# Kernel optimization log

Hardware: AMD Instinct MI355X
Metric: run time of the kernel (lower is better)

The kernel has to match this reference:

```python
import jax, jax.numpy as jnp
import numpy as np

B, C, H = 64, 64, 32

def _pm_cross_pairs(ks):
    # Replicates PM_cross(2, ks): pairs (i, i+j) ordered by gap j=1..ks-1, then i.
    a, b = [], []
    for j in range(1, ks):
        for i in range(ks - j):
            a.append(i)
            b.append(i + j)
    return np.array(a, dtype=np.int32), np.array(b, dtype=np.int32)

def setup_inputs() -> dict:
    key = jax.random.key(0)
    k1, k2 = jax.random.split(key)
    ia, ib = _pm_cross_pairs(H)           # 496 pairs for H=32
    hk = ia.shape[0] + 2 * H              # 560
    x = jax.random.normal(k1, (B, C, H, H), dtype=jnp.float32)
    weight = 0.1 * jax.random.normal(k2, (C, H, hk, H), dtype=jnp.float32)
    return {"x": x, "weight": weight, "idx_a": jnp.asarray(ia), "idx_b": jnp.asarray(ib)}

def reference(x, weight, idx_a, idx_b):
    # cross-term products along last axis: [B,C,H,P]
    cross = x[..., idx_a] * x[..., idx_b]
    feat = jnp.concatenate([x, x * x, cross], axis=-1)  # [B,C,H,Hk]
    # per-(channel,row) grouped matmul
    return jnp.einsum('bcij,cijo->bcio', feat, weight)
```

## Files before the change

kernel.cpp:

```cpp
#include <hip/hip_runtime.h>

#define NB 64
#define NC 64
#define NH 32
#define HK 560
#define NOCT 88
#define NCHUNK 11
#define XSTR 57

typedef __bf16 bf16x8 __attribute__((ext_vector_type(8)));
typedef float f32x4 __attribute__((ext_vector_type(4)));

__global__ __launch_bounds__(256, 5) void hconv_kernel(
    const float* __restrict__ x, const float* __restrict__ w,
    const int* __restrict__ idx_a, const int* __restrict__ idx_b,
    float* __restrict__ out)
{
    __shared__ float s_x[NB * XSTR];
    __shared__ unsigned s_desc[NOCT];

    const int t = threadIdx.x;
    const int g = blockIdx.x;
    const int c = g >> 5, i = g & 31;

    {
        const int xrow = t >> 2, seg = t & 3;
        const float* xr = x + (((size_t)xrow * NC + c) * NH + i) * NH + seg * 8;
        float4 v0 = *(const float4*)(xr);
        float4 v1 = *(const float4*)(xr + 4);
        float* dst = &s_x[xrow * XSTR + 8 + seg * 8];
        dst[0] = v0.x; dst[1] = v0.y; dst[2] = v0.z; dst[3] = v0.w;
        dst[4] = v1.x; dst[5] = v1.y; dst[6] = v1.z; dst[7] = v1.w;
        if (seg == 0) {
            float* r0 = &s_x[xrow * XSTR];
            #pragma unroll
            for (int m = 0; m < 8; ++m) {
                r0[m] = 0.0f;
                r0[40 + m] = 0.0f;
                r0[48 + m] = 1.0f;
            }
        }
    }

    if (t < NOCT) {
        unsigned pa, pb, ko;
        if (t < 4)      { pa = 8u + 8u * t; pb = 48u; ko = 8u * t; }
        else if (t < 8) { unsigned u = t - 4; pa = pb = 8u + 8u * u; ko = 32u + 8u * u; }
        else if (t < 84) {
            unsigned q = t - 8, j, a;
            if (q < 28)      { j = 1 + q / 4;         a = q % 4; }
            else if (q < 52) { j = 8 + (q - 28) / 3;  a = (q - 28) % 3; }
            else if (q < 68) { j = 16 + (q - 52) / 2; a = (q - 52) % 2; }
            else             { j = 24 + (q - 68);     a = 0; }
            ko = 64u + (j - 1) * 32u - (j * (j - 1)) / 2u + 8u * a;
            pa = 8u + 8u * a; pb = pa + j;
            if (ko > 552u) { unsigned s = ko - 552u; ko = 552u; pa -= s; pb -= s; }
        } else { pa = 0u; pb = 0u; ko = 0u; }
        s_desc[t] = pa | (pb << 6) | (ko << 12);
    }

    const int wv = t >> 6, lane = t & 63;
    const int lr = lane & 15, lq = lane >> 4;
    const int arow = wv * 16 + lr;
    const float* wbase = w + (size_t)(c * NH + i) * HK * NH;
    const float* xrp = &s_x[arow * XSTR];

    __syncthreads();

    f32x4 acc0 = {0.f, 0.f, 0.f, 0.f};
    f32x4 acc1 = {0.f, 0.f, 0.f, 0.f};

    unsigned d0 = s_desc[lq];
    unsigned d1 = s_desc[4 + lq];

    for (int ch = 0; ch < NCHUNK; ++ch) {
        unsigned nd0 = 0, nd1 = 0;
        if (ch + 1 < NCHUNK) {
            nd0 = s_desc[(ch + 1) * 8 + lq];
            nd1 = s_desc[(ch + 1) * 8 + 4 + lq];
        }
        const unsigned pa0 = d0 & 63u, pb0 = (d0 >> 6) & 63u, ko0 = d0 >> 12;
        const unsigned pa1 = d1 & 63u, pb1 = (d1 >> 6) & 63u, ko1 = d1 >> 12;

        const float* wb0 = wbase + (size_t)ko0 * NH + lr;
        const float* wb1 = wbase + (size_t)ko1 * NH + lr;
        float b0v[8], b1v[8], b2v[8], b3v[8];
        #pragma unroll
        for (int j = 0; j < 8; ++j) {
            b0v[j] = wb0[j * NH];
            b1v[j] = wb0[j * NH + 16];
            b2v[j] = wb1[j * NH];
            b3v[j] = wb1[j * NH + 16];
        }

        const float* pA0 = xrp + pa0; const float* pB0 = xrp + pb0;
        const float* pA1 = xrp + pa1; const float* pB1 = xrp + pb1;
        bf16x8 a0, a1;
        #pragma unroll
        for (int j = 0; j < 8; ++j) {
            a0[j] = (__bf16)(pA0[j] * pB0[j]);
            a1[j] = (__bf16)(pA1[j] * pB1[j]);
        }

        bf16x8 f0, f1, f2, f3;
        #pragma unroll
        for (int j = 0; j < 8; ++j) {
            f0[j] = (__bf16)b0v[j]; f1[j] = (__bf16)b1v[j];
            f2[j] = (__bf16)b2v[j]; f3[j] = (__bf16)b3v[j];
        }

        acc0 = __builtin_amdgcn_mfma_f32_16x16x32_bf16(a0, f0, acc0, 0, 0, 0);
        acc1 = __builtin_amdgcn_mfma_f32_16x16x32_bf16(a0, f1, acc1, 0, 0, 0);
        acc0 = __builtin_amdgcn_mfma_f32_16x16x32_bf16(a1, f2, acc0, 0, 0, 0);
        acc1 = __builtin_amdgcn_mfma_f32_16x16x32_bf16(a1, f3, acc1, 0, 0, 0);

        d0 = nd0; d1 = nd1;
    }

    #pragma unroll
    for (int r = 0; r < 4; ++r) {
        const int b = wv * 16 + lq * 4 + r;
        float* op = out + (((size_t)b * NC + c) * NH + i) * NH;
        op[lr] = acc0[r];
        op[16 + lr] = acc1[r];
    }
}

extern "C" void kernel_launch(void* const* d_in, const int* in_sizes, int n_in,
                              void* d_out, int out_size, void* d_ws, size_t ws_size,
                              hipStream_t stream) {
    const float* x = (const float*)d_in[0];
    const float* w = (const float*)d_in[1];
    const int* idx_a = (const int*)d_in[2];
    const int* idx_b = (const int*)d_in[3];
    float* out = (float*)d_out;
    hconv_kernel<<<dim3(NC * NH), dim3(256), 0, stream>>>(x, w, idx_a, idx_b, out);
}
```

Before: 240.8 us.

## Stage weights cooperatively in double-buffered LDS as bf16 shared across waves

Previously each of the four waves loaded the same weight slice from global memory and converted it to bf16 on its own. Now the block loads each weight chunk once, cooperatively, converts it to bf16 and stores it transposed in a double-buffered LDS tile, with the next chunk's global loads prefetched into registers while the current chunk is fed to the MFMAs. The chunk count is padded from 11 to 12 so the loop can run in pairs; the extra chunk uses zero activations and adds no contribution. The change cuts redundant global traffic and conversion work, at the cost of extra LDS use, a wasted chunk and two block barriers per iteration pair.

```diff
diff --git a/kernel.cpp b/kernel.cpp
--- a/kernel.cpp
+++ b/kernel.cpp
@@ -4,8 +4,8 @@
 #define NC 64
 #define NH 32
 #define HK 560
-#define NOCT 88
-#define NCHUNK 11
+#define NOCT 96
+#define NCHUNK 12
 #define XSTR 57
 
 typedef __bf16 bf16x8 __attribute__((ext_vector_type(8)));
@@ -18,6 +18,7 @@
 {
     __shared__ float s_x[NB * XSTR];
     __shared__ unsigned s_desc[NOCT];
+    __shared__ __align__(16) unsigned short s_wT[2][32][72];
 
     const int t = threadIdx.x;
     const int g = blockIdx.x;
@@ -62,59 +63,66 @@
     const int wv = t >> 6, lane = t & 63;
     const int lr = lane & 15, lq = lane >> 4;
     const int arow = wv * 16 + lr;
+    const int wo = t & 31;
+    const int wkg = t >> 5;
     const float* wbase = w + (size_t)(c * NH + i) * HK * NH;
     const float* xrp = &s_x[arow * XSTR];
 
     __syncthreads();
 
+    unsigned sd[NCHUNK];
+    #pragma unroll
+    for (int ch = 0; ch < NCHUNK; ++ch) sd[ch] = s_desc[ch * 8 + wkg] >> 12;
+
+    float p0[8], p1[8];
+
+    auto wload = [&](int ch, float* pv) {
+        const float* p = wbase + (size_t)sd[ch] * NH + wo;
+        #pragma unroll
+        for (int r = 0; r < 8; ++r) pv[r] = p[r * NH];
+    };
+    auto wstore = [&](int bufi, const float* pv) {
+        bf16x8 v;
+        #pragma unroll
+        for (int r = 0; r < 8; ++r) v[r] = (__bf16)pv[r];
+        *(bf16x8*)&s_wT[bufi][wo][wkg * 8] = v;
+    };
+
     f32x4 acc0 = {0.f, 0.f, 0.f, 0.f};
     f32x4 acc1 = {0.f, 0.f, 0.f, 0.f};
 
-    unsigned d0 = s_desc[lq];
-    unsigned d1 = s_desc[4 + lq];
+    auto mfma_chunk = [&](int ch, int bufi) {
+        #pragma unroll
+        for (int ks = 0; ks < 2; ++ks) {
+            const unsigned d = s_desc[ch * 8 + ks * 4 + lq];
+            const float* pA = xrp + (d & 63u);
+            const float* pB = xrp + ((d >> 6) & 63u);
+            bf16x8 a;
+            #pragma unroll
+            for (int j = 0; j < 8; ++j)
+                a[j] = (__bf16)(pA[j] * pB[j]);
+            bf16x8 b0 = *(const bf16x8*)&s_wT[bufi][lr][ks * 32 + lq * 8];
+            bf16x8 b1 = *(const bf16x8*)&s_wT[bufi][16 + lr][ks * 32 + lq * 8];
+            acc0 = __builtin_amdgcn_mfma_f32_16x16x32_bf16(a, b0, acc0, 0, 0, 0);
+            acc1 = __builtin_amdgcn_mfma_f32_16x16x32_bf16(a, b1, acc1, 0, 0, 0);
+        }
+    };
 
-    for (int ch = 0; ch < NCHUNK; ++ch) {
-        unsigned nd0 = 0, nd1 = 0;
-        if (ch + 1 < NCHUNK) {
-            nd0 = s_desc[(ch + 1) * 8 + lq];
-            nd1 = s_desc[(ch + 1) * 8 + 4 + lq];
-        }
-        const unsigned pa0 = d0 & 63u, pb0 = (d0 >> 6) & 63u, ko0 = d0 >> 12;
-        const unsigned pa1 = d1 & 63u, pb1 = (d1 >> 6) & 63u, ko1 = d1 >> 12;
+    wload(0, p0);
+    wload(1, p1);
+    wstore(0, p0);
+    __syncthreads();
 
-        const float* wb0 = wbase + (size_t)ko0 * NH + lr;
-        const float* wb1 = wbase + (size_t)ko1 * NH + lr;
-        float b0v[8], b1v[8], b2v[8], b3v[8];
-        #pragma unroll
-        for (int j = 0; j < 8; ++j) {
-            b0v[j] = wb0[j * NH];
-            b1v[j] = wb0[j * NH + 16];
-            b2v[j] = wb1[j * NH];
-            b3v[j] = wb1[j * NH + 16];
-        }
-
-        const float* pA0 = xrp + pa0; const float* pB0 = xrp + pb0;
-        const float* pA1 = xrp + pa1; const float* pB1 = xrp + pb1;
-        bf16x8 a0, a1;
-        #pragma unroll
-        for (int j = 0; j < 8; ++j) {
-            a0[j] = (__bf16)(pA0[j] * pB0[j]);
-            a1[j] = (__bf16)(pA1[j] * pB1[j]);
-        }
-
-        bf16x8 f0, f1, f2, f3;
-        #pragma unroll
-        for (int j = 0; j < 8; ++j) {
-            f0[j] = (__bf16)b0v[j]; f1[j] = (__bf16)b1v[j];
-            f2[j] = (__bf16)b2v[j]; f3[j] = (__bf16)b3v[j];
-        }
-
-        acc0 = __builtin_amdgcn_mfma_f32_16x16x32_bf16(a0, f0, acc0, 0, 0, 0);
-        acc1 = __builtin_amdgcn_mfma_f32_16x16x32_bf16(a0, f1, acc1, 0, 0, 0);
-        acc0 = __builtin_amdgcn_mfma_f32_16x16x32_bf16(a1, f2, acc0, 0, 0, 0);
-        acc1 = __builtin_amdgcn_mfma_f32_16x16x32_bf16(a1, f3, acc1, 0, 0, 0);
-
-        d0 = nd0; d1 = nd1;
+    for (int it = 0; it < 6; ++it) {
+        const int ca = 2 * it, cb = 2 * it + 1;
+        wload(ca + 2 < NCHUNK ? ca + 2 : NCHUNK - 1, p0);
+        mfma_chunk(ca, 0);
+        wstore(1, p1);
+        __syncthreads();
+        wload(cb + 2 < NCHUNK ? cb + 2 : NCHUNK - 1, p1);
+        mfma_chunk(cb, 1);
+        wstore(0, p0);
+        __syncthreads();
     }
 
     #pragma unroll
```

After: 232.4 us. 1.04x faster.

## Double-buffer weight loads in registers across unrolled chunk pairs

Applied to the files above, without the earlier changes.

Restructures the chunk loop into a two-stage register pipeline. Weights for chunk n+2 are loaded while chunks n and n+1 are consumed by MFMA, so global load latency overlaps with compute. To make the unroll-by-two even, the chunk count is padded to 12 using zero descriptors. Those padded chunks read zero x columns, so they contribute nothing to the result but cost redundant loads and MFMAs. The occupancy hint drops from 5 to 4 blocks per CU to make room for the extra 64 prefetch registers.

```diff
diff --git a/kernel.cpp b/kernel.cpp
--- a/kernel.cpp
+++ b/kernel.cpp
@@ -4,14 +4,14 @@
 #define NC 64
 #define NH 32
 #define HK 560
-#define NOCT 88
-#define NCHUNK 11
+#define NOCT 96
+#define NCHUNK 12
 #define XSTR 57
 
 typedef __bf16 bf16x8 __attribute__((ext_vector_type(8)));
 typedef float f32x4 __attribute__((ext_vector_type(4)));
 
-__global__ __launch_bounds__(256, 5) void hconv_kernel(
+__global__ __launch_bounds__(256, 4) void hconv_kernel(
     const float* __restrict__ x, const float* __restrict__ w,
     const int* __restrict__ idx_a, const int* __restrict__ idx_b,
     float* __restrict__ out)
@@ -70,51 +70,63 @@
     f32x4 acc0 = {0.f, 0.f, 0.f, 0.f};
     f32x4 acc1 = {0.f, 0.f, 0.f, 0.f};
 
-    unsigned d0 = s_desc[lq];
-    unsigned d1 = s_desc[4 + lq];
-
-    for (int ch = 0; ch < NCHUNK; ++ch) {
-        unsigned nd0 = 0, nd1 = 0;
-        if (ch + 1 < NCHUNK) {
-            nd0 = s_desc[(ch + 1) * 8 + lq];
-            nd1 = s_desc[(ch + 1) * 8 + 4 + lq];
-        }
-        const unsigned pa0 = d0 & 63u, pb0 = (d0 >> 6) & 63u, ko0 = d0 >> 12;
-        const unsigned pa1 = d1 & 63u, pb1 = (d1 >> 6) & 63u, ko1 = d1 >> 12;
-
-        const float* wb0 = wbase + (size_t)ko0 * NH + lr;
-        const float* wb1 = wbase + (size_t)ko1 * NH + lr;
-        float b0v[8], b1v[8], b2v[8], b3v[8];
+    auto bload = [&](int ch, unsigned& d0, unsigned& d1, float* pv) {
+        d0 = s_desc[ch * 8 + lq];
+        d1 = s_desc[ch * 8 + 4 + lq];
+        const float* w0 = wbase + (size_t)(d0 >> 12) * NH + lr;
+        const float* w1 = wbase + (size_t)(d1 >> 12) * NH + lr;
         #pragma unroll
         for (int j = 0; j < 8; ++j) {
-            b0v[j] = wb0[j * NH];
-            b1v[j] = wb0[j * NH + 16];
-            b2v[j] = wb1[j * NH];
-            b3v[j] = wb1[j * NH + 16];
+            pv[j]      = w0[j * NH];
+            pv[8 + j]  = w0[j * NH + 16];
+            pv[16 + j] = w1[j * NH];
+            pv[24 + j] = w1[j * NH + 16];
         }
+    };
 
-        const float* pA0 = xrp + pa0; const float* pB0 = xrp + pb0;
-        const float* pA1 = xrp + pa1; const float* pB1 = xrp + pb1;
-        bf16x8 a0, a1;
+    auto abuild = [&](unsigned d) -> bf16x8 {
+        const float* pA = xrp + (d & 63u);
+        const float* pB = xrp + ((d >> 6) & 63u);
+        bf16x8 a;
         #pragma unroll
-        for (int j = 0; j < 8; ++j) {
-            a0[j] = (__bf16)(pA0[j] * pB0[j]);
-            a1[j] = (__bf16)(pA1[j] * pB1[j]);
-        }
+        for (int j = 0; j < 8; ++j)
+            a[j] = (__bf16)(pA[j] * pB[j]);
+        return a;
+    };
 
+    auto consume = [&](unsigned d0, unsigned d1, const float* pv) {
+        bf16x8 a0 = abuild(d0);
+        bf16x8 a1 = abuild(d1);
         bf16x8 f0, f1, f2, f3;
         #pragma unroll
         for (int j = 0; j < 8; ++j) {
-            f0[j] = (__bf16)b0v[j]; f1[j] = (__bf16)b1v[j];
-            f2[j] = (__bf16)b2v[j]; f3[j] = (__bf16)b3v[j];
+            f0[j] = (__bf16)pv[j];      f1[j] = (__bf16)pv[8 + j];
+            f2[j] = (__bf16)pv[16 + j]; f3[j] = (__bf16)pv[24 + j];
         }
-
         acc0 = __builtin_amdgcn_mfma_f32_16x16x32_bf16(a0, f0, acc0, 0, 0, 0);
         acc1 = __builtin_amdgcn_mfma_f32_16x16x32_bf16(a0, f1, acc1, 0, 0, 0);
         acc0 = __builtin_amdgcn_mfma_f32_16x16x32_bf16(a1, f2, acc0, 0, 0, 0);
         acc1 = __builtin_amdgcn_mfma_f32_16x16x32_bf16(a1, f3, acc1, 0, 0, 0);
+    };
 
-        d0 = nd0; d1 = nd1;
+    unsigned dA0, dA1, dB0, dB1;
+    float pvA[32], pvB[32];
+    bload(0, dA0, dA1, pvA);
+    bload(1, dB0, dB1, pvB);
+
+    #pragma unroll
+    for (int it = 0; it < 6; ++it) {
+        const int ca = 2 * it, cb = 2 * it + 1;
+        consume(dA0, dA1, pvA);
+        {
+            const int nc = (ca + 2 < NCHUNK) ? ca + 2 : NCHUNK - 1;
+            bload(nc, dA0, dA1, pvA);
+        }
+        consume(dB0, dB1, pvB);
+        {
+            const int nc = (cb + 2 < NCHUNK) ? cb + 2 : NCHUNK - 1;
+            bload(nc, dB0, dB1, pvB);
+        }
     }
 
     #pragma unroll
```

Result: no change. 238.9 us (-0.8%).
